# Kernel tuning notes

Measured on AMD Instinct MI355X. Metric: run time of the kernel, lower is better.

The kernel has to match this reference:

```python
import jax, jax.numpy as jnp
import numpy as np

B, S, E, HEADS = 2, 2048, 2048, 16


def setup_inputs() -> dict:
    key = jax.random.key(0)
    k1, k2, k3 = jax.random.split(key, 3)
    x = jax.random.normal(k1, (B, S, E), dtype=jnp.float32)
    # Linear weights stored as (in, out); torch uses y = x @ W.T with W (out, in) -- same math.
    W_qkvh = jax.random.normal(k2, (E, 3 * E + HEADS), dtype=jnp.float32) * (E ** -0.5)
    W_out = jax.random.normal(k3, (E, E), dtype=jnp.float32) * (E ** -0.5)
    return {"x": x, "W_qkvh": W_qkvh, "W_out": W_out}


def reference(x, W_qkvh, W_out):
    b, s, e = x.shape
    heads = W_qkvh.shape[1] - 3 * e
    d = e // heads
    scale = e ** 0.5

    proj = x @ W_qkvh                                  # (b, s, 3e + heads)
    QKV, Hg = proj[..., : 3 * e], proj[..., 3 * e:]
    Hg = jnp.tanh(Hg).transpose(0, 2, 1)[..., None]    # (b, h, s, 1) gate
    QKV = QKV.reshape(b, s, heads, 3 * d).transpose(0, 2, 1, 3)  # (b, h, s, 3d)
    Q, K, V = jnp.split(QKV, 3, axis=-1)               # each (b, h, s, d)

    # Cummean(H*K) along seq: cumsum(n * x) / n^2 with n = 1..s
    n = jnp.arange(1, s + 1, dtype=x.dtype).reshape(1, 1, s, 1)
    Kc = jnp.cumsum(n * (Hg * K), axis=2) / (n * n)    # (b, h, s, d)

    scores = jnp.einsum('bhqd,bhkd->bhqk', Q, Kc) / scale
    causal = jnp.triu(jnp.ones((s, s), dtype=bool), k=1)
    scores = jnp.where(causal, -jnp.inf, scores)
    attn = jax.nn.softmax(scores, axis=-1)

    out = jnp.einsum('bhqk,bhkd->bhqd', attn, V)       # (b, h, s, d)
    out = out.transpose(0, 2, 1, 3).reshape(b, s, e)
    return out @ W_out
```

## Files before the change

kernel.cpp:

```cpp
#include <hip/hip_runtime.h>
#include <hip/hip_bf16.h>
#include <math.h>

#define PB 2
#define PS 2048
#define PE 2048
#define PH 16
#define PD 128
#define PN_PROJ 6160
#define PM 4096
#define PQKV 6144

typedef __attribute__((ext_vector_type(8))) short bf16x8;
typedef __attribute__((ext_vector_type(4))) float f32x4;

__device__ __forceinline__ void gload_lds16(const void* g, void* l) {
  __builtin_amdgcn_global_load_lds((const __attribute__((address_space(1))) void*)g,
                                   (__attribute__((address_space(3))) void*)l, 16, 0, 0);
}

template <int BM, int BN, int WM, int WN, typename OutT>
__global__ __launch_bounds__(WM * WN * 64, 2) void gemm_8p(
    const __hip_bfloat16* __restrict__ A, const __hip_bfloat16* __restrict__ Bt,
    OutT* __restrict__ C, int K, int lda, int ldb, int ldc, int nTilesX) {
  constexpr int BK = 64;
  constexpr int T = WM * WN * 64;
  constexpr int AR = BM * BK * 2 / (T * 16);
  constexpr int BR = BN * BK * 2 / (T * 16);
  constexpr int NLD = AR + BR;
  constexpr int MF = BM / WM / 16;
  constexpr int NF = BN / WN / 16;
  constexpr int BUFE = (BM + BN) * BK;

  __shared__ __align__(16) __hip_bfloat16 smem[2 * BUFE];

  const int tid = threadIdx.x;
  const int w = tid >> 6, lane = tid & 63;
  const int fq = lane >> 4, fr = lane & 15;
  const int wm = w / WN, wn = w % WN;

  const int total = gridDim.x;
  const int swz = (blockIdx.x & 7) * (total >> 3) + (blockIdx.x >> 3);
  const int mBase = (swz / nTilesX) * BM;
  const int nBase = (swz % nTilesX) * BN;

  auto stage = [&](int t, int buf) {
    char* ab = (char*)smem + (size_t)buf * BUFE * 2;
    char* bb = ab + BM * BK * 2;
    const int wub = tid & ~63;
#pragma unroll
    for (int p = 0; p < AR; ++p) {
      int g = p * T + tid;
      int row = g >> 3, c = g & 7;
      int cs = c ^ (row & 7);
      gload_lds16(A + (size_t)(mBase + row) * lda + t * BK + cs * 8,
                  ab + (size_t)(p * T + wub) * 16);
    }
#pragma unroll
    for (int p = 0; p < BR; ++p) {
      int g = p * T + tid;
      int row = g >> 3, c = g & 7;
      int cs = c ^ (row & 7);
      gload_lds16(Bt + (size_t)(nBase + row) * ldb + t * BK + cs * 8,
                  bb + (size_t)(p * T + wub) * 16);
    }
  };

  f32x4 acc[MF][NF];
#pragma unroll
  for (int m = 0; m < MF; ++m)
#pragma unroll
    for (int n = 0; n < NF; ++n) acc[m][n] = (f32x4){0.f, 0.f, 0.f, 0.f};

  const int NT = K / BK;
  stage(0, 0);
  stage(1, 1);

#pragma unroll 1
  for (int t = 0; t < NT; ++t) {
    if (t + 1 < NT) asm volatile("s_waitcnt vmcnt(%0)" ::"i"(NLD) : "memory");
    else            asm volatile("s_waitcnt vmcnt(0)" ::: "memory");
    __builtin_amdgcn_s_barrier();
    __builtin_amdgcn_sched_barrier(0);

    const __hip_bfloat16* As = smem + (size_t)(t & 1) * BUFE;
    const __hip_bfloat16* Bs = As + BM * BK;

#pragma unroll
    for (int mh = 0; mh < MF / 4; ++mh) {
      bf16x8 av[4][2];
#pragma unroll
      for (int m = 0; m < 4; ++m)
#pragma unroll
        for (int kk = 0; kk < 2; ++kk) {
          int row = wm * (BM / WM) + (mh * 4 + m) * 16 + fr;
          av[m][kk] = *(const bf16x8*)&As[row * BK + (((kk * 4 + fq) ^ (row & 7)) * 8)];
        }
#pragma unroll
      for (int nh = 0; nh < NF / 2; ++nh) {
        bf16x8 bv[2][2];
#pragma unroll
        for (int n = 0; n < 2; ++n)
#pragma unroll
          for (int kk = 0; kk < 2; ++kk) {
            int row = wn * (BN / WN) + (nh * 2 + n) * 16 + fr;
            bv[n][kk] = *(const bf16x8*)&Bs[row * BK + (((kk * 4 + fq) ^ (row & 7)) * 8)];
          }
        __builtin_amdgcn_s_setprio(1);
#pragma unroll
        for (int m = 0; m < 4; ++m)
#pragma unroll
          for (int n = 0; n < 2; ++n)
#pragma unroll
            for (int kk = 0; kk < 2; ++kk)
              acc[mh * 4 + m][nh * 2 + n] = __builtin_amdgcn_mfma_f32_16x16x32_bf16(
                  av[m][kk], bv[n][kk], acc[mh * 4 + m][nh * 2 + n], 0, 0, 0);
        __builtin_amdgcn_s_setprio(0);
      }
    }

    __builtin_amdgcn_sched_barrier(0);
    asm volatile("s_waitcnt lgkmcnt(0)" ::: "memory");
    __builtin_amdgcn_s_barrier();
    if (t + 2 < NT) stage(t + 2, t & 1);
  }

#pragma unroll
  for (int m = 0; m < MF; ++m) {
#pragma unroll
    for (int n = 0; n < NF; ++n) {
      int row0 = mBase + wm * (BM / WM) + m * 16 + fq * 4;
      int col = nBase + wn * (BN / WN) + n * 16 + fr;
#pragma unroll
      for (int j = 0; j < 4; ++j) {
        if constexpr (__is_same(OutT, float))
          C[(size_t)(row0 + j) * ldc + col] = acc[m][n][j];
        else
          C[(size_t)(row0 + j) * ldc + col] = __float2bfloat16(acc[m][n][j]);
      }
    }
  }
}

__global__ __launch_bounds__(256) void cast_f32_bf16(const float* __restrict__ in,
                                                     __hip_bfloat16* __restrict__ out,
                                                     int n4) {
  int i = blockIdx.x * 256 + threadIdx.x;
  if (i >= n4) return;
  float4 v = ((const float4*)in)[i];
  union { __hip_bfloat16 h[4]; uint2 u; } pk;
  pk.h[0] = __float2bfloat16(v.x); pk.h[1] = __float2bfloat16(v.y);
  pk.h[2] = __float2bfloat16(v.z); pk.h[3] = __float2bfloat16(v.w);
  ((uint2*)out)[i] = pk.u;
}

__global__ __launch_bounds__(256) void transpose_cast(const float* __restrict__ W,
                                                      __hip_bfloat16* __restrict__ Wt,
                                                      int ldw, int ldt, int nOff) {
  __shared__ float t[32][33];
  int nb = blockIdx.x * 32, kb = blockIdx.y * 32;
  int tx = threadIdx.x & 31, ty = threadIdx.x >> 5;
#pragma unroll
  for (int i = 0; i < 4; ++i) {
    int k = ty + i * 8;
    t[k][tx] = W[(size_t)(kb + k) * ldw + nOff + nb + tx];
  }
  __syncthreads();
#pragma unroll
  for (int i = 0; i < 4; ++i) {
    int n = ty + i * 8;
    Wt[(size_t)(nb + n) * ldt + kb + tx] = __float2bfloat16(t[tx][n]);
  }
}

__global__ __launch_bounds__(256) void hg_from_x(const float* __restrict__ x,
                                                 const float* __restrict__ W,
                                                 float* __restrict__ hgbuf) {
  int bs = blockIdx.x;
  int b = bs >> 11, s = bs & (PS - 1);
  __shared__ float xs[PE];
  __shared__ float red[16][17];
  const float* xr = x + (size_t)bs * PE;
  for (int i = threadIdx.x; i < PE / 4; i += 256)
    *(float4*)&xs[i * 4] = ((const float4*)xr)[i];
  __syncthreads();
  int h = threadIdx.x & 15, part = threadIdx.x >> 4;
  float acc = 0.f;
  for (int k = part * 128; k < part * 128 + 128; ++k)
    acc += xs[k] * W[(size_t)k * PN_PROJ + 3 * PE + h];
  red[part][h] = acc;
  __syncthreads();
  if (threadIdx.x < 16) {
    float sm = 0.f;
#pragma unroll
    for (int p = 0; p < 16; ++p) sm += red[p][threadIdx.x];
    hgbuf[(size_t)(b * PH + threadIdx.x) * PS + s] = tanhf(sm);
  }
}

#define KC_SCALE 0.022097086912079608f

__global__ __launch_bounds__(128) void kc_pass1(const __hip_bfloat16* __restrict__ proj,
                                                const float* __restrict__ hgbuf,
                                                float* __restrict__ csum) {
  int c = blockIdx.x & 15, bh = blockIdx.x >> 4;
  int h = bh & (PH - 1), b = bh >> 4;
  int d = threadIdx.x;
  __shared__ float hgs[128];
  hgs[d] = hgbuf[bh * PS + c * 128 + d];
  __syncthreads();
  const __hip_bfloat16* kbase = proj + (size_t)(b * PS) * PQKV + h * 384 + 128 + d;
  float acc = 0.f;
  int j0 = c * 128;
  for (int i = 0; i < 128; ++i) {
    int j = j0 + i;
    acc += (float)(j + 1) * hgs[i] * __bfloat162float(kbase[(size_t)j * PQKV]);
  }
  csum[blockIdx.x * 128 + d] = acc;
}

__global__ __launch_bounds__(128) void kc_pass2(__hip_bfloat16* __restrict__ proj,
                                                const float* __restrict__ hgbuf,
                                                const float* __restrict__ csum) {
  int c = blockIdx.x & 15, bh = blockIdx.x >> 4;
  int h = bh & (PH - 1), b = bh >> 4;
  int d = threadIdx.x;
  __shared__ float hgs[128];
  hgs[d] = hgbuf[bh * PS + c * 128 + d];
  __syncthreads();
  float acc = 0.f;
  for (int cc = 0; cc < c; ++cc) acc += csum[(bh * 16 + cc) * 128 + d];
  __hip_bfloat16* kbase = proj + (size_t)(b * PS) * PQKV + h * 384 + 128 + d;
  int j0 = c * 128;
  for (int i = 0; i < 128; ++i) {
    int j = j0 + i;
    acc += (float)(j + 1) * hgs[i] * __bfloat162float(kbase[(size_t)j * PQKV]);
    float t = (float)(j + 1);
    kbase[(size_t)j * PQKV] = __float2bfloat16(acc / (t * t) * KC_SCALE);
  }
}

__global__ __launch_bounds__(256) void vt_pack(const __hip_bfloat16* __restrict__ proj,
                                               __hip_bfloat16* __restrict__ Vtp) {
  int sc = blockIdx.x & 31, bh = blockIdx.x >> 5;
  int b = bh >> 4, h = bh & 15;
  int s0 = sc * 64;
  int tid = threadIdx.x;
  __shared__ __align__(16) __hip_bfloat16 Vlds[64][136];
  const __hip_bfloat16* src = proj + (size_t)(b * PS + s0) * PQKV + h * 384 + 256;
#pragma unroll
  for (int it = 0; it < 4; ++it) {
    int i = it * 256 + tid;
    int row = i >> 4, ch = i & 15;
    *(bf16x8*)&Vlds[row][ch * 8] = *(const bf16x8*)&src[(size_t)row * PQKV + ch * 8];
  }
  __syncthreads();
  int d = tid >> 1, half = tid & 1;
  __hip_bfloat16* dst = Vtp + ((size_t)bh * 128 + d) * PS + s0 + half * 32;
#pragma unroll
  for (int c8 = 0; c8 < 8; ++c8) {
    union { __hip_bfloat16 h4[4]; uint2 u; } pk;
#pragma unroll
    for (int k = 0; k < 4; ++k) pk.h4[k] = Vlds[half * 32 + c8 * 4 + k][d];
    *(uint2*)&dst[c8 * 4] = pk.u;
  }
}

__global__ __launch_bounds__(256) void attn_mfma(const __hip_bfloat16* __restrict__ proj,
                                                 const __hip_bfloat16* __restrict__ Vtp,
                                                 __hip_bfloat16* __restrict__ O) {
  const int bid = (blockIdx.x & 7) * 32 + (blockIdx.x >> 3);
  const int bh = bid >> 3, pk = bid & 7;
  const int b = bh >> 4, h = bh & 15;
  const int tid = threadIdx.x;
  const int w = tid >> 6, lane = tid & 63;
  const int fq = lane >> 4, fr = lane & 15;

  __shared__ __align__(16) char smem[120832];
  __hip_bfloat16* Psw = (__hip_bfloat16*)(smem + 65536) + w * 32 * 72;
  __hip_bfloat16* Os = (__hip_bfloat16*)(smem + 84480);

  const __hip_bfloat16* kb0 = proj + (size_t)(b * PS) * PQKV + h * 384 + 128;
  const __hip_bfloat16* vb0 = Vtp + (size_t)bh * 128 * PS;

  const int klr = lane >> 4, kc = lane & 15;
  const int vlr = lane >> 3, vc = lane & 7;

  auto stageKV = [&](int t, int bufi) {
    char* ksb = smem + bufi * 16384;
    char* vsb = smem + 32768 + bufi * 16384;
    const __hip_bfloat16* kb = kb0 + (size_t)(t * 64) * PQKV;
    const __hip_bfloat16* vb = vb0 + t * 64;
#pragma unroll
    for (int p = 0; p < 4; ++p) {
      int row = w * 16 + p * 4 + klr;
      int cs = kc ^ (row & 7);
      gload_lds16(kb + (size_t)row * PQKV + cs * 8, ksb + (w * 16 + p * 4) * 256);
    }
#pragma unroll
    for (int p = 0; p < 4; ++p) {
      int row = w * 32 + p * 8 + vlr;
      int cs = vc ^ (row & 7);
      gload_lds16(vb + (size_t)row * PS + cs * 8, vsb + (w * 32 + p * 8) * 128);
    }
  };

  stageKV(0, 0);
  int cur = 0;

#pragma unroll 1
  for (int phase = 0; phase < 2; ++phase) {
    const int qt = (phase == 0) ? pk : 15 - pk;
    const int nt = (qt + 1) * 2;
    const int q0 = qt * 128;
    const int qw = q0 + w * 32;

    const __hip_bfloat16* qbase = proj + (size_t)(b * PS + qw) * PQKV + h * 384;
    bf16x8 qf[2][4];
#pragma unroll
    for (int r2 = 0; r2 < 2; ++r2)
#pragma unroll
      for (int kk = 0; kk < 4; ++kk)
        qf[r2][kk] = *(const bf16x8*)&qbase[(size_t)(r2 * 16 + fr) * PQKV + kk * 32 + fq * 8];

    f32x4 oacc[2][8];
#pragma unroll
    for (int r2 = 0; r2 < 2; ++r2)
#pragma unroll
      for (int nd = 0; nd < 8; ++nd) oacc[r2][nd] = (f32x4){0.f, 0.f, 0.f, 0.f};
    float m_[2] = {-__builtin_inff(), -__builtin_inff()};
    float l_[2] = {0.f, 0.f};

#pragma unroll 1
    for (int kt = 0; kt < nt; ++kt) {
      const bool hasNext = (kt + 1 < nt) || (phase == 0);
      if (hasNext) stageKV((kt + 1 < nt) ? kt + 1 : 0, cur ^ 1);

      if (kt * 64 <= qw + 31) {
        const __hip_bfloat16* Ks = (const __hip_bfloat16*)(smem + cur * 16384);
        const __hip_bfloat16* Vts = (const __hip_bfloat16*)(smem + 32768 + cur * 16384);
        const bool diag = (kt * 64 + 63) > qw;

        f32x4 sacc[2][4];
#pragma unroll
        for (int r2 = 0; r2 < 2; ++r2)
#pragma unroll
          for (int n = 0; n < 4; ++n) sacc[r2][n] = (f32x4){0.f, 0.f, 0.f, 0.f};
#pragma unroll
        for (int kk = 0; kk < 4; ++kk) {
#pragma unroll
          for (int n = 0; n < 4; ++n) {
            bf16x8 kf = *(const bf16x8*)&Ks[(n * 16 + fr) * 128 + (((kk * 4 + fq) ^ (fr & 7)) * 8)];
            sacc[0][n] = __builtin_amdgcn_mfma_f32_16x16x32_bf16(kf, qf[0][kk], sacc[0][n], 0, 0, 0);
            sacc[1][n] = __builtin_amdgcn_mfma_f32_16x16x32_bf16(kf, qf[1][kk], sacc[1][n], 0, 0, 0);
          }
        }

#pragma unroll
        for (int r2 = 0; r2 < 2; ++r2) {
          const int qg = qw + r2 * 16 + fr;
          float sv[4][4];
#pragma unroll
          for (int n = 0; n < 4; ++n)
#pragma unroll
            for (int j = 0; j < 4; ++j) {
              float s = sacc[r2][n][j];
              if (diag && (kt * 64 + n * 16 + fq * 4 + j) > qg) s = -__builtin_inff();
              sv[n][j] = s;
            }
          float pmax = sv[0][0];
#pragma unroll
          for (int n = 0; n < 4; ++n)
#pragma unroll
            for (int j = 0; j < 4; ++j) pmax = fmaxf(pmax, sv[n][j]);
          pmax = fmaxf(pmax, __shfl_xor(pmax, 16, 64));
          pmax = fmaxf(pmax, __shfl_xor(pmax, 32, 64));

          const bool nof = __all(pmax <= m_[r2] + 8.f);
          const float mn = nof ? m_[r2] : fmaxf(m_[r2], pmax);
          float ps = 0.f;
#pragma unroll
          for (int n = 0; n < 4; ++n) {
            union { __hip_bfloat16 hh[4]; uint2 u; } pkk;
#pragma unroll
            for (int j = 0; j < 4; ++j) {
              float p = __expf(sv[n][j] - mn);
              ps += p;
              pkk.hh[j] = __float2bfloat16(p);
            }
            *(uint2*)&Psw[(r2 * 16 + fr) * 72 + n * 16 + fq * 4] = pkk.u;
          }
          ps += __shfl_xor(ps, 16, 64);
          ps += __shfl_xor(ps, 32, 64);

          if (!nof) {
            const float alpha = __expf(m_[r2] - mn);
            l_[r2] = l_[r2] * alpha + ps;
            m_[r2] = mn;
            float a0 = __shfl(alpha, fq * 4 + 0, 64);
            float a1 = __shfl(alpha, fq * 4 + 1, 64);
            float a2 = __shfl(alpha, fq * 4 + 2, 64);
            float a3 = __shfl(alpha, fq * 4 + 3, 64);
#pragma unroll
            for (int nd = 0; nd < 8; ++nd) {
              oacc[r2][nd][0] *= a0; oacc[r2][nd][1] *= a1;
              oacc[r2][nd][2] *= a2; oacc[r2][nd][3] *= a3;
            }
          } else {
            l_[r2] += ps;
          }
        }

#pragma unroll
        for (int kk2 = 0; kk2 < 2; ++kk2) {
          bf16x8 pa0 = *(const bf16x8*)&Psw[(0 * 16 + fr) * 72 + kk2 * 32 + fq * 8];
          bf16x8 pa1 = *(const bf16x8*)&Psw[(1 * 16 + fr) * 72 + kk2 * 32 + fq * 8];
#pragma unroll
          for (int nd = 0; nd < 8; ++nd) {
            bf16x8 vf = *(const bf16x8*)&Vts[(nd * 16 + fr) * 64 + (((kk2 * 4 + fq) ^ (fr & 7)) * 8)];
            oacc[0][nd] = __builtin_amdgcn_mfma_f32_16x16x32_bf16(pa0, vf, oacc[0][nd], 0, 0, 0);
            oacc[1][nd] = __builtin_amdgcn_mfma_f32_16x16x32_bf16(pa1, vf, oacc[1][nd], 0, 0, 0);
          }
        }
      }

      __syncthreads();
      cur ^= 1;
    }

    float i0 = 1.0f / l_[0], i1 = 1.0f / l_[1];
    float inv4[2][4];
#pragma unroll
    for (int j = 0; j < 4; ++j) {
      inv4[0][j] = __shfl(i0, fq * 4 + j, 64);
      inv4[1][j] = __shfl(i1, fq * 4 + j, 64);
    }
#pragma unroll
    for (int r2 = 0; r2 < 2; ++r2)
#pragma unroll
      for (int nd = 0; nd < 8; ++nd)
#pragma unroll
        for (int j = 0; j < 4; ++j)
          Os[(w * 32 + r2 * 16 + fq * 4 + j) * 136 + nd * 16 + fr] =
              __float2bfloat16(oacc[r2][nd][j] * inv4[r2][j]);
    __syncthreads();
#pragma unroll
    for (int it = 0; it < 8; ++it) {
      int i = it * 256 + tid;
      int row = i >> 4, ch = i & 15;
      *(bf16x8*)&O[(size_t)(b * PS + q0 + row) * PE + h * 128 + ch * 8] =
          *(const bf16x8*)&Os[row * 136 + ch * 8];
    }
  }
}

extern "C" void kernel_launch(void* const* d_in, const int* in_sizes, int n_in,
                              void* d_out, int out_size, void* d_ws, size_t ws_size,
                              hipStream_t stream) {
  const float* x     = (const float*)d_in[0];
  const float* Wqkvh = (const float*)d_in[1];
  const float* Wout  = (const float*)d_in[2];
  float* out = (float*)d_out;

  char* wsb = (char*)d_ws;
  __hip_bfloat16* proj = (__hip_bfloat16*)wsb;
  wsb += (size_t)PM * PQKV * 2;
  __hip_bfloat16* xb = (__hip_bfloat16*)wsb;
  wsb += (size_t)PM * PE * 2;
  __hip_bfloat16* Wq_t = (__hip_bfloat16*)wsb;
  wsb += (size_t)PQKV * PE * 2;
  __hip_bfloat16* Wout_t = (__hip_bfloat16*)wsb;
  wsb += (size_t)PE * PE * 2;
  __hip_bfloat16* Vtp = (__hip_bfloat16*)wsb;
  wsb += (size_t)PB * PH * PD * PS * 2;
  float* hgbuf = (float*)wsb;
  wsb += (size_t)PB * PH * PS * 4;
  float* csum = (float*)wsb;

  cast_f32_bf16<<<(PM * PE / 4 + 255) / 256, 256, 0, stream>>>(x, xb, PM * PE / 4);
  transpose_cast<<<dim3(PQKV / 32, PE / 32), 256, 0, stream>>>(Wqkvh, Wq_t, PN_PROJ, PE, 0);
  transpose_cast<<<dim3(PE / 32, PE / 32), 256, 0, stream>>>(Wout, Wout_t, PE, PE, 0);

  gemm_8p<256, 256, 2, 4, __hip_bfloat16><<<dim3((PQKV / 256) * (PM / 256)), 512, 0, stream>>>(
      xb, Wq_t, proj, PE, PE, PE, PQKV, PQKV / 256);

  hg_from_x<<<PM, 256, 0, stream>>>(x, Wqkvh, hgbuf);
  kc_pass1<<<PB * PH * 16, 128, 0, stream>>>(proj, hgbuf, csum);
  kc_pass2<<<PB * PH * 16, 128, 0, stream>>>(proj, hgbuf, csum);

  vt_pack<<<PB * PH * 32, 256, 0, stream>>>(proj, Vtp);
  __hip_bfloat16* Ob = xb;
  attn_mfma<<<PB * PH * 8, 256, 0, stream>>>(proj, Vtp, Ob);

  gemm_8p<128, 256, 1, 8, float><<<dim3((PE / 256) * (PM / 128)), 512, 0, stream>>>(
      Ob, Wout_t, out, PE, PE, PE, PE, PE / 256);
}
```

Baseline: 348.3 us.

## Rewrite GEMM with 4-stage K=32 chunk pipeline and 128x256 tiles

Replaces the double-buffered BK=64 GEMM with a four-buffer ring of K=32 chunks that keeps three loads in flight. Each iteration loads its fragments, issues the next chunk's global-to-LDS copy, then runs one 16-MFMA phase, which drops the second barrier per step. Both projection GEMMs now use 128x256 tiles with a 2x4 wave layout and launch bounds of one block per CU. The aim is to hide memory latency better and use finer tiles for the QKV GEMM, at the cost of more barriers per unit of K and possibly lower occupancy.

```diff
diff --git a/kernel.cpp b/kernel.cpp
--- a/kernel.cpp
+++ b/kernel.cpp
@@ -20,19 +20,17 @@
 }
 
 template <int BM, int BN, int WM, int WN, typename OutT>
-__global__ __launch_bounds__(WM * WN * 64, 2) void gemm_8p(
+__global__ __launch_bounds__(512, 1) void gemm_cs(
     const __hip_bfloat16* __restrict__ A, const __hip_bfloat16* __restrict__ Bt,
     OutT* __restrict__ C, int K, int lda, int ldb, int ldc, int nTilesX) {
-  constexpr int BK = 64;
-  constexpr int T = WM * WN * 64;
-  constexpr int AR = BM * BK * 2 / (T * 16);
-  constexpr int BR = BN * BK * 2 / (T * 16);
-  constexpr int NLD = AR + BR;
   constexpr int MF = BM / WM / 16;
   constexpr int NF = BN / WN / 16;
-  constexpr int BUFE = (BM + BN) * BK;
-
-  __shared__ __align__(16) __hip_bfloat16 smem[2 * BUFE];
+  static_assert(MF * NF == 16, "one 16-MFMA phase per chunk");
+  constexpr int SBE = (BM + BN) * 32;
+  constexpr int AL = BM / 128;
+  constexpr int BL = BN / 128;
+
+  __shared__ __align__(16) __hip_bfloat16 lds[4 * SBE];
 
   const int tid = threadIdx.x;
   const int w = tid >> 6, lane = tid & 63;
@@ -44,25 +42,23 @@
   const int mBase = (swz / nTilesX) * BM;
   const int nBase = (swz % nTilesX) * BN;
 
-  auto stage = [&](int t, int buf) {
-    char* ab = (char*)smem + (size_t)buf * BUFE * 2;
-    char* bb = ab + BM * BK * 2;
-    const int wub = tid & ~63;
-#pragma unroll
-    for (int p = 0; p < AR; ++p) {
-      int g = p * T + tid;
-      int row = g >> 3, c = g & 7;
-      int cs = c ^ (row & 7);
-      gload_lds16(A + (size_t)(mBase + row) * lda + t * BK + cs * 8,
-                  ab + (size_t)(p * T + wub) * 16);
-    }
-#pragma unroll
-    for (int p = 0; p < BR; ++p) {
-      int g = p * T + tid;
-      int row = g >> 3, c = g & 7;
-      int cs = c ^ (row & 7);
-      gload_lds16(Bt + (size_t)(nBase + row) * ldb + t * BK + cs * 8,
-                  bb + (size_t)(p * T + wub) * 16);
+  const int srow = tid >> 2, sc = tid & 3;
+
+  auto stage_chunk = [&](int u) {
+    char* base = (char*)lds + (size_t)(u & 3) * SBE * 2;
+#pragma unroll
+    for (int l = 0; l < AL; ++l) {
+      int row = l * 128 + srow;
+      int cs = sc ^ (row & 3);
+      gload_lds16(A + (size_t)(mBase + row) * lda + u * 32 + cs * 8,
+                  base + l * 8192 + w * 1024);
+    }
+#pragma unroll
+    for (int l = 0; l < BL; ++l) {
+      int row = l * 128 + srow;
+      int cs = sc ^ (row & 3);
+      gload_lds16(Bt + (size_t)(nBase + row) * ldb + u * 32 + cs * 8,
+                  base + BM * 64 + l * 8192 + w * 1024);
     }
   };
 
@@ -72,57 +68,59 @@
 #pragma unroll
     for (int n = 0; n < NF; ++n) acc[m][n] = (f32x4){0.f, 0.f, 0.f, 0.f};
 
-  const int NT = K / BK;
-  stage(0, 0);
-  stage(1, 1);
+  const int NC = K / 32;
+  stage_chunk(0); stage_chunk(1); stage_chunk(2);
 
 #pragma unroll 1
-  for (int t = 0; t < NT; ++t) {
-    if (t + 1 < NT) asm volatile("s_waitcnt vmcnt(%0)" ::"i"(NLD) : "memory");
-    else            asm volatile("s_waitcnt vmcnt(0)" ::: "memory");
+  for (int u = 0; u < NC - 2; ++u) {
+    asm volatile("s_waitcnt vmcnt(6)" ::: "memory");
     __builtin_amdgcn_s_barrier();
     __builtin_amdgcn_sched_barrier(0);
-
-    const __hip_bfloat16* As = smem + (size_t)(t & 1) * BUFE;
-    const __hip_bfloat16* Bs = As + BM * BK;
-
-#pragma unroll
-    for (int mh = 0; mh < MF / 4; ++mh) {
-      bf16x8 av[4][2];
-#pragma unroll
-      for (int m = 0; m < 4; ++m)
-#pragma unroll
-        for (int kk = 0; kk < 2; ++kk) {
-          int row = wm * (BM / WM) + (mh * 4 + m) * 16 + fr;
-          av[m][kk] = *(const bf16x8*)&As[row * BK + (((kk * 4 + fq) ^ (row & 7)) * 8)];
-        }
-#pragma unroll
-      for (int nh = 0; nh < NF / 2; ++nh) {
-        bf16x8 bv[2][2];
-#pragma unroll
-        for (int n = 0; n < 2; ++n)
-#pragma unroll
-          for (int kk = 0; kk < 2; ++kk) {
-            int row = wn * (BN / WN) + (nh * 2 + n) * 16 + fr;
-            bv[n][kk] = *(const bf16x8*)&Bs[row * BK + (((kk * 4 + fq) ^ (row & 7)) * 8)];
-          }
-        __builtin_amdgcn_s_setprio(1);
-#pragma unroll
-        for (int m = 0; m < 4; ++m)
-#pragma unroll
-          for (int n = 0; n < 2; ++n)
-#pragma unroll
-            for (int kk = 0; kk < 2; ++kk)
-              acc[mh * 4 + m][nh * 2 + n] = __builtin_amdgcn_mfma_f32_16x16x32_bf16(
-                  av[m][kk], bv[n][kk], acc[mh * 4 + m][nh * 2 + n], 0, 0, 0);
-        __builtin_amdgcn_s_setprio(0);
-      }
-    }
-
+    const __hip_bfloat16* sl = lds + (size_t)(u & 3) * SBE;
+    bf16x8 av[MF], bv[NF];
+#pragma unroll
+    for (int m = 0; m < MF; ++m) {
+      int row = wm * (BM / WM) + m * 16 + fr;
+      av[m] = *(const bf16x8*)&sl[row * 32 + ((fq ^ (row & 3)) * 8)];
+    }
+#pragma unroll
+    for (int n = 0; n < NF; ++n) {
+      int row = wn * (BN / WN) + n * 16 + fr;
+      bv[n] = *(const bf16x8*)&sl[BM * 32 + row * 32 + ((fq ^ (row & 3)) * 8)];
+    }
+    if (u + 3 < NC) stage_chunk(u + 3);
+    asm volatile("s_waitcnt lgkmcnt(0)" ::: "memory");
     __builtin_amdgcn_sched_barrier(0);
-    asm volatile("s_waitcnt lgkmcnt(0)" ::: "memory");
-    __builtin_amdgcn_s_barrier();
-    if (t + 2 < NT) stage(t + 2, t & 1);
+    __builtin_amdgcn_s_setprio(1);
+#pragma unroll
+    for (int m = 0; m < MF; ++m)
+#pragma unroll
+      for (int n = 0; n < NF; ++n)
+        acc[m][n] = __builtin_amdgcn_mfma_f32_16x16x32_bf16(av[m], bv[n], acc[m][n], 0, 0, 0);
+    __builtin_amdgcn_s_setprio(0);
+  }
+
+  asm volatile("s_waitcnt vmcnt(0)" ::: "memory");
+  __builtin_amdgcn_s_barrier();
+#pragma unroll 1
+  for (int u = NC - 2; u < NC; ++u) {
+    const __hip_bfloat16* sl = lds + (size_t)(u & 3) * SBE;
+    bf16x8 av[MF], bv[NF];
+#pragma unroll
+    for (int m = 0; m < MF; ++m) {
+      int row = wm * (BM / WM) + m * 16 + fr;
+      av[m] = *(const bf16x8*)&sl[row * 32 + ((fq ^ (row & 3)) * 8)];
+    }
+#pragma unroll
+    for (int n = 0; n < NF; ++n) {
+      int row = wn * (BN / WN) + n * 16 + fr;
+      bv[n] = *(const bf16x8*)&sl[BM * 32 + row * 32 + ((fq ^ (row & 3)) * 8)];
+    }
+#pragma unroll
+    for (int m = 0; m < MF; ++m)
+#pragma unroll
+      for (int n = 0; n < NF; ++n)
+        acc[m][n] = __builtin_amdgcn_mfma_f32_16x16x32_bf16(av[m], bv[n], acc[m][n], 0, 0, 0);
   }
 
 #pragma unroll
@@ -481,8 +479,9 @@
   transpose_cast<<<dim3(PQKV / 32, PE / 32), 256, 0, stream>>>(Wqkvh, Wq_t, PN_PROJ, PE, 0);
   transpose_cast<<<dim3(PE / 32, PE / 32), 256, 0, stream>>>(Wout, Wout_t, PE, PE, 0);
 
-  gemm_8p<256, 256, 2, 4, __hip_bfloat16><<<dim3((PQKV / 256) * (PM / 256)), 512, 0, stream>>>(
-      xb, Wq_t, proj, PE, PE, PE, PQKV, PQKV / 256);
+  gemm_cs<128, 256, 2, 4, __hip_bfloat16>
+      <<<dim3((PM / 128) * (PQKV / 256)), 512, 0, stream>>>(
+          xb, Wq_t, proj, PE, PE, PE, PQKV, PQKV / 256);
 
   hg_from_x<<<PM, 256, 0, stream>>>(x, Wqkvh, hgbuf);
   kc_pass1<<<PB * PH * 16, 128, 0, stream>>>(proj, hgbuf, csum);
@@ -492,6 +491,7 @@
   __hip_bfloat16* Ob = xb;
   attn_mfma<<<PB * PH * 8, 256, 0, stream>>>(proj, Vtp, Ob);
 
-  gemm_8p<128, 256, 1, 8, float><<<dim3((PE / 256) * (PM / 128)), 512, 0, stream>>>(
-      Ob, Wout_t, out, PE, PE, PE, PE, PE / 256);
-}
+  gemm_cs<128, 256, 2, 4, float>
+      <<<dim3((PM / 128) * (PE / 256)), 512, 0, stream>>>(
+          Ob, Wout_t, out, PE, PE, PE, PE, PE / 256);
+}
```

After: 336.3 us. -3.5%, faster.
